# Performance work log

Hardware: AMD Instinct MI355X
Metric: run time of the kernel (lower is better)

## Reference

```python
import jax, jax.numpy as jnp
import numpy as np

SEGMENT_LENGTHS = [1024, 4096]
DILATION_RATES = [1, 2]
HILBERT_CHUNK = 4096
B, N, H, D = 2, 4096, 16, 64


def _hilbert_mapping(n: int) -> np.ndarray:
    """Replicates _generate_hilbert_curve: gather indices for a length-n chunk."""
    if n <= 64:
        return np.arange(n, dtype=np.int64)
    size = 1
    while size * size < n:
        size *= 2

    def d2xy(nn, d):
        x = y = 0
        s = 1
        while s < nn:
            rx = 1 if (d // 2) & 1 else 0
            ry = 1 if (d ^ rx) & 1 else 0
            if ry == 0:
                if rx == 1:
                    x, y = nn - 1 - x, nn - 1 - y
                x, y = y, x
            x += s * rx
            y += s * ry
            d //= 4
            s *= 2
        return x, y

    mapping = np.zeros(n, dtype=np.int64)
    h2l = {}
    for i in range(min(n, size * size)):
        x, y = d2xy(size, i)
        li = y * size + x
        if li < n:
            h2l[i] = li
    hidx = 0
    for i in sorted(h2l):
        mapping[h2l[i]] = hidx
        hidx += 1
    return mapping


def _apply_hilbert(t: jnp.ndarray) -> jnp.ndarray:
    # t: [b, n, h, d]; reorder sequence within HILBERT_CHUNK-sized chunks.
    n = t.shape[1]
    chunks = []
    for start in range(0, n, HILBERT_CHUNK):
        end = min(start + HILBERT_CHUNK, n)
        m = jnp.asarray(_hilbert_mapping(end - start))
        chunks.append(t[:, start:end][:, m])
    return jnp.concatenate(chunks, axis=1) if len(chunks) > 1 else chunks[0]


def _dilation_indices(s: int, r: int, offset: int) -> np.ndarray:
    # Replicates _create_dilation_pattern
    idx = np.arange(offset, s, r, dtype=np.int64)
    expected = (s + r - 1 - offset) // r
    if idx.shape[0] > expected:
        idx = idx[:expected]
    elif idx.shape[0] < expected:
        pad = np.arange(expected - idx.shape[0], dtype=np.int64) % idx.shape[0]
        idx = np.concatenate([idx, idx[pad]])
    return idx


def _dilated_attention(q, k, v):
    # LongNet-style dilated attention: heads partitioned across groups;
    # each group attends within segments over dilated positions.
    b, n, h, d = q.shape
    G = len(SEGMENT_LENGTHS)
    hg = h // G
    scale = 1.0 / np.sqrt(d).astype(np.float32)
    out = jnp.zeros_like(q)
    for g, (s, r) in enumerate(zip(SEGMENT_LENGTHS, DILATION_RATES)):
        offset = g % r
        idx = jnp.asarray(_dilation_indices(s, r, offset))
        hs = slice(g * hg, (g + 1) * hg)
        # [b, n//s, s, hg, d] -> dilated [b, n//s, s/r, hg, d]
        qg = q[:, :, hs].reshape(b, n // s, s, hg, d)[:, :, idx]
        kg = k[:, :, hs].reshape(b, n // s, s, hg, d)[:, :, idx]
        vg = v[:, :, hs].reshape(b, n // s, s, hg, d)[:, :, idx]
        att = jnp.einsum('bgqhd,bgkhd->bghqk', qg, kg) * scale
        att = jax.nn.softmax(att, axis=-1)
        og = jnp.einsum('bghqk,bgkhd->bgqhd', att, vg)
        full = jnp.zeros((b, n // s, s, hg, d), q.dtype).at[:, :, idx].set(og)
        out = out.at[:, :, hs].set(full.reshape(b, n, hg, d))
    return out


def setup_inputs() -> dict:
    key = jax.random.key(0)
    kq, kk, kv = jax.random.split(key, 3)
    q = jax.random.normal(kq, (B, N, H, D), dtype=jnp.float32)
    k = jax.random.normal(kk, (B, N, H, D), dtype=jnp.float32)
    v = jax.random.normal(kv, (B, N, H, D), dtype=jnp.float32)
    return {'q': q, 'k': k, 'v': v}


def reference(q, k, v):
    k_h = _apply_hilbert(k)
    v_h = _apply_hilbert(v)
    return _dilated_attention(q, k_h, v_h)
```

## Files before the change

### kernel.cpp

```cpp
#include <hip/hip_runtime.h>
#include <hip/hip_bf16.h>

#define N_ 4096
#define H_ 16
#define D_ 64
#define G1ROWOFF 65536

typedef __attribute__((ext_vector_type(4))) float f32x4;
typedef __attribute__((ext_vector_type(8))) _Float16 f16x8;

#define AS1 __attribute__((address_space(1)))
#define AS3 __attribute__((address_space(3)))

__device__ __forceinline__ unsigned int pkrtz(float a, float b){
  auto h = __builtin_amdgcn_cvt_pkrtz(a, b);
  unsigned int r; __builtin_memcpy(&r, &h, 4); return r;
}
__device__ __forceinline__ unsigned int pku(unsigned int lo, unsigned int hi){
  return lo | (hi << 16);
}

__global__ __launch_bounds__(1024) void hilbert_map_kernel(int* __restrict__ mapping){
  __shared__ int sm[4096];
  const int t = threadIdx.x;
#pragma unroll
  for(int jj=0;jj<4;jj++) mapping[t*4+jj] = 0;
  int li_a[4], val_a[4];
#pragma unroll
  for(int jj=0;jj<4;jj++){
    int i = t*4+jj;
    int x=0,y=0,d=i;
#pragma unroll
    for(int s=1;s<64;s<<=1){
      int rx=(d>>1)&1;
      int ry=(d^rx)&1;
      if(ry==0){
        if(rx==1){ x=63-x; y=63-y; }
        int tp=x; x=y; y=tp;
      }
      x+=s*rx; y+=s*ry;
      d>>=2;
    }
    int li=y*64+x;
    li_a[jj]=li;
    val_a[jj]=(li<4096)?1:0;
    sm[i]=val_a[jj];
  }
  __syncthreads();
  for(int off=1;off<4096;off<<=1){
    int v[4];
#pragma unroll
    for(int jj=0;jj<4;jj++){
      int i=t*4+jj;
      v[jj]=sm[i]+((i>=off)?sm[i-off]:0);
    }
    __syncthreads();
#pragma unroll
    for(int jj=0;jj<4;jj++) sm[t*4+jj]=v[jj];
    __syncthreads();
  }
#pragma unroll
  for(int jj=0;jj<4;jj++){
    if(val_a[jj]){
      int rank=sm[t*4+jj]-1;
      int li=li_a[jj];
      int wi=(li>=0)?li:(4096+li);
      if(wi>=0 && wi<4096) atomicMax(&mapping[wi], rank);
    }
  }
}

__global__ __launch_bounds__(256) void prep_kv_kernel(
    const float* __restrict__ K, const float* __restrict__ V,
    const int* __restrict__ hmap,
    unsigned short* __restrict__ Kh, unsigned short* __restrict__ Vt)
{
  __shared__ unsigned short Vlds[64*72];
  const int bid = blockIdx.x, tid = threadIdx.x;
  int b, h, dstRowBase, srcRow;
  const int r = tid>>2, part = tid&3;
  if (bid < 1024){
    int t64 = bid&63; h = (bid>>6)&7; b = bid>>9;
    dstRowBase = (b*8+h)*4096 + t64*64;
    srcRow = t64*64 + r;
  } else {
    int bid2 = bid-1024;
    int t64 = bid2&31; int h8 = (bid2>>5)&7; b = bid2>>8; h = 8+h8;
    dstRowBase = G1ROWOFF + (b*8+h8)*2048 + t64*64;
    srcRow = 1 + 2*(t64*64 + r);
  }
  const int src = hmap[srcRow];
  const size_t sb = (((size_t)(b*N_+src))*H_ + h)*D_ + part*16;
  {
    const float4* kp = (const float4*)(K + sb);
    float4 a=kp[0], c=kp[1], e=kp[2], g=kp[3];
    uint4 w0, w1;
    w0.x=pkrtz(a.x,a.y); w0.y=pkrtz(a.z,a.w); w0.z=pkrtz(c.x,c.y); w0.w=pkrtz(c.z,c.w);
    w1.x=pkrtz(e.x,e.y); w1.y=pkrtz(e.z,e.w); w1.z=pkrtz(g.x,g.y); w1.w=pkrtz(g.z,g.w);
    char* dst = (char*)Kh + ((size_t)(dstRowBase+r))*128;
    *(uint4*)(dst + ((2*part  )^(r&7))*16) = w0;
    *(uint4*)(dst + ((2*part+1)^(r&7))*16) = w1;
  }
  {
    const float4* vp = (const float4*)(V + sb);
    float4 a=vp[0], c=vp[1], e=vp[2], g=vp[3];
    uint4 w0, w1;
    w0.x=pkrtz(a.x,a.y); w0.y=pkrtz(a.z,a.w); w0.z=pkrtz(c.x,c.y); w0.w=pkrtz(c.z,c.w);
    w1.x=pkrtz(e.x,e.y); w1.y=pkrtz(e.z,e.w); w1.z=pkrtz(g.x,g.y); w1.w=pkrtz(g.z,g.w);
    uint4* dst=(uint4*)&Vlds[r*72 + part*16];
    dst[0]=w0; dst[1]=w1;
  }
  __syncthreads();
  {
    const int d = tid>>2, p2 = tid&3;
    unsigned int w0[4], w1[4];
#pragma unroll
    for(int c=0;c<2;c++){
      int kb = 32*c + 4*p2;
      unsigned int* w = c ? w1 : w0;
      w[0] = pku(Vlds[(kb+ 0)*72+d], Vlds[(kb+ 1)*72+d]);
      w[1] = pku(Vlds[(kb+ 2)*72+d], Vlds[(kb+ 3)*72+d]);
      w[2] = pku(Vlds[(kb+16)*72+d], Vlds[(kb+17)*72+d]);
      w[3] = pku(Vlds[(kb+18)*72+d], Vlds[(kb+19)*72+d]);
    }
    char* dst = (char*)Vt + ((size_t)(dstRowBase+d))*128;
    *(uint4*)(dst + ((p2  )^(d&7))*16) = *(uint4*)w0;
    *(uint4*)(dst + ((p2+4)^(d&7))*16) = *(uint4*)w1;
  }
}

__global__ __launch_bounds__(256, 2) void dilated_attn_kernel(
    const float* __restrict__ Q, const unsigned short* __restrict__ Kh,
    const unsigned short* __restrict__ Vt, float* __restrict__ Out)
{
  __shared__ __align__(16) char smem[65536];

  const int bid = blockIdx.x, tid = threadIdx.x;
  const int wave = tid>>6, lane = tid&63;
  const int lr = lane&15, lg = lane>>4;

  int b, outH, qstep, qoff, njobs, nrj;
  int qloc[2];
  size_t kb0, kb1;
  if (bid < 256){
    int xcd = bid&7, idx = bid>>3;
    int kblk = idx&15, Hp = idx>>4;
    int H = xcd + 8*Hp;
    b = H>>3; outH = 8 + (H&7);
    qstep = 2; qoff = 1; njobs = 1; nrj = 16;
    qloc[0] = kblk*128; qloc[1] = qloc[0];
    size_t rowBase = (size_t)G1ROWOFF + (size_t)H*2048;
    kb0 = rowBase*128; kb1 = kb0 + 16*8192;
    int i = tid>>1, half = tid&1;
    int zpos = 2*(qloc[0] + i);
    float4 z = {0.f,0.f,0.f,0.f};
    float4* op = (float4*)(Out + (((size_t)(b*N_+zpos))*H_ + outH)*D_ + half*32);
#pragma unroll
    for(int j=0;j<8;j++) op[j]=z;
  } else {
    int p = bid - 256;
    int xcd = p&7, idx = p>>3;
    int pair = idx&3, Gp = idx>>2;
    int G = xcd + 8*Gp;
    b = G>>5; int seg=(G>>3)&3; int h=G&7; outH=h;
    qstep = 1; qoff = 0; njobs = 2; nrj = 8;
    qloc[0] = seg*1024 + pair*128;
    qloc[1] = seg*1024 + (pair+4)*128;
    size_t rowBase = ((size_t)(b*8+h))*4096 + (size_t)seg*1024;
    kb0 = rowBase*128; kb1 = kb0;
  }

  const float SCL = 0.125f * 1.4426950408889634f;
  f16x8 qf[2][2];
  f32x4 acc[2][4];
  f32x4 accl[2];
  const f32x4 FZ = {0.f,0.f,0.f,0.f};
  union{ unsigned int u[4]; f16x8 v; } ONES;
  ONES.u[0]=0x3C003C00u; ONES.u[1]=0x3C003C00u; ONES.u[2]=0x3C003C00u; ONES.u[3]=0x3C003C00u;

  auto loadQ = [&](int ql0){
#pragma unroll
    for(int qs=0;qs<2;qs++){
      int qpos = qoff + qstep*(ql0 + wave*32 + qs*16 + lr);
      const float* qp = Q + (((size_t)(b*N_+qpos))*H_ + outH)*D_;
#pragma unroll
      for(int dc=0;dc<2;dc++){
        float4 a = *(const float4*)(qp + dc*32 + lg*8);
        float4 c = *(const float4*)(qp + dc*32 + lg*8 + 4);
        union{ unsigned int u[4]; f16x8 v; } pk;
        pk.u[0]=pkrtz(a.x*SCL,a.y*SCL); pk.u[1]=pkrtz(a.z*SCL,a.w*SCL);
        pk.u[2]=pkrtz(c.x*SCL,c.y*SCL); pk.u[3]=pkrtz(c.z*SCL,c.w*SCL);
        qf[qs][dc]=pk.v;
      }
    }
  };

  const int swz = lr&7;
  const int kA0 = lr*128 + ((  lg)^swz)*16;
  const int kA1 = lr*128 + ((4+lg)^swz)*16;
  const int vA0 = 8192 + lr*128 + ((  lg)^swz)*16;
  const int vA1 = 8192 + lr*128 + ((4+lg)^swz)*16;

  const char* gBase = (wave<2) ? (const char*)Kh : (const char*)Vt;
  const int sOff = (tid&127)*16;
  const int sHalf = (wave<2) ? 0 : 8192;
  auto stage = [&](int bufOff, int t){
    size_t off = ((t>=16)? kb1 : kb0) + (size_t)(t&15)*8192 + sOff;
    const char* gsrc = gBase + off;
    char* ldst = smem + bufOff + sHalf + sOff;
#pragma unroll
    for(int i=0;i<4;i++){
      __builtin_amdgcn_global_load_lds((const AS1 void*)(gsrc + i*2048),
                                       (AS3 void*)(ldst + i*2048), 16, 0, 0);
    }
  };

  auto epilogue = [&](int ql0){
#pragma unroll
    for(int qs=0;qs<2;qs++)
#pragma unroll
      for(int r=0;r<4;r++){
        float inv = 1.0f/accl[qs][r];
        int qpos = qoff + qstep*(ql0 + wave*32 + qs*16 + lg*4 + r);
        float* op = Out + (((size_t)(b*N_+qpos))*H_ + outH)*D_ + lr;
#pragma unroll
        for(int dt=0;dt<4;dt++) op[dt*16] = acc[qs][dt][r]*inv;
      }
  };

  stage(0, 0); stage(16384, 1);
  int p = 0;
  for(int j=0; j<njobs; ++j){
    loadQ(qloc[j]);
#pragma unroll
    for(int qs=0;qs<2;qs++){
#pragma unroll
      for(int dt=0;dt<4;dt++) acc[qs][dt] = FZ;
      accl[qs] = FZ;
    }
    for(int r=0; r<nrj; ++r, ++p){
      asm volatile("s_waitcnt vmcnt(0)" ::: "memory");
      __builtin_amdgcn_s_barrier();
      const int half = (p&1)*32768;
      if (p < 15){
        const int oth = ((p+1)&1)*32768;
        stage(oth, 2*p+2); stage(oth+16384, 2*p+3);
      }
      const char* smA = smem + half;
      const char* smB = smem + half + 16384;

      f32x4 sA[2][4], sB[2][4];
#pragma unroll
      for(int kt=0;kt<4;kt++){
        f16x8 k0 = *(const f16x8*)(smA + kA0 + kt*2048);
        f16x8 k1 = *(const f16x8*)(smA + kA1 + kt*2048);
#pragma unroll
        for(int qs=0;qs<2;qs++){
          sA[qs][kt] = __builtin_amdgcn_mfma_f32_16x16x32_f16(k0, qf[qs][0], FZ, 0,0,0);
          sA[qs][kt] = __builtin_amdgcn_mfma_f32_16x16x32_f16(k1, qf[qs][1], sA[qs][kt],0,0,0);
        }
      }

      unsigned int UA[2][4][2], UB[2][4][2];
#pragma unroll
      for(int kt=0;kt<4;kt++){
        f16x8 k0 = *(const f16x8*)(smB + kA0 + kt*2048);
        f16x8 k1 = *(const f16x8*)(smB + kA1 + kt*2048);
        sB[0][kt] = __builtin_amdgcn_mfma_f32_16x16x32_f16(k0, qf[0][0], FZ, 0,0,0);
        UA[0][kt][0] = pkrtz(__builtin_amdgcn_exp2f(sA[0][kt][0]),
                             __builtin_amdgcn_exp2f(sA[0][kt][1]));
        sB[0][kt] = __builtin_amdgcn_mfma_f32_16x16x32_f16(k1, qf[0][1], sB[0][kt],0,0,0);
        UA[0][kt][1] = pkrtz(__builtin_amdgcn_exp2f(sA[0][kt][2]),
                             __builtin_amdgcn_exp2f(sA[0][kt][3]));
        sB[1][kt] = __builtin_amdgcn_mfma_f32_16x16x32_f16(k0, qf[1][0], FZ, 0,0,0);
        UA[1][kt][0] = pkrtz(__builtin_amdgcn_exp2f(sA[1][kt][0]),
                             __builtin_amdgcn_exp2f(sA[1][kt][1]));
        sB[1][kt] = __builtin_amdgcn_mfma_f32_16x16x32_f16(k1, qf[1][1], sB[1][kt],0,0,0);
        UA[1][kt][1] = pkrtz(__builtin_amdgcn_exp2f(sA[1][kt][2]),
                             __builtin_amdgcn_exp2f(sA[1][kt][3]));
      }
      union{ unsigned int u[4]; f16x8 v; } pfA[2][2];
#pragma unroll
      for(int qs=0;qs<2;qs++)
#pragma unroll
        for(int c=0;c<2;c++){
          pfA[qs][c].u[0]=UA[qs][2*c][0]; pfA[qs][c].u[1]=UA[qs][2*c][1];
          pfA[qs][c].u[2]=UA[qs][2*c+1][0]; pfA[qs][c].u[3]=UA[qs][2*c+1][1];
        }

#pragma unroll
      for(int c=0;c<2;c++){
        const int vAc = c ? vA1 : vA0;
#pragma unroll
        for(int dt=0;dt<4;dt++){
          f16x8 vf = *(const f16x8*)(smA + vAc + dt*2048);
          const int bqs = dt>>1, bkt = 2*c + (dt&1);
          acc[0][dt] = __builtin_amdgcn_mfma_f32_16x16x32_f16(pfA[0][c].v, vf, acc[0][dt],0,0,0);
          UB[bqs][bkt][0] = pkrtz(__builtin_amdgcn_exp2f(sB[bqs][bkt][0]),
                                  __builtin_amdgcn_exp2f(sB[bqs][bkt][1]));
          acc[1][dt] = __builtin_amdgcn_mfma_f32_16x16x32_f16(pfA[1][c].v, vf, acc[1][dt],0,0,0);
          UB[bqs][bkt][1] = pkrtz(__builtin_amdgcn_exp2f(sB[bqs][bkt][2]),
                                  __builtin_amdgcn_exp2f(sB[bqs][bkt][3]));
        }
        accl[0] = __builtin_amdgcn_mfma_f32_16x16x32_f16(pfA[0][c].v, ONES.v, accl[0],0,0,0);
        accl[1] = __builtin_amdgcn_mfma_f32_16x16x32_f16(pfA[1][c].v, ONES.v, accl[1],0,0,0);
      }

#pragma unroll
      for(int c=0;c<2;c++){
        union{ unsigned int u[4]; f16x8 v; } pf0, pf1;
        pf0.u[0]=UB[0][2*c][0]; pf0.u[1]=UB[0][2*c][1]; pf0.u[2]=UB[0][2*c+1][0]; pf0.u[3]=UB[0][2*c+1][1];
        pf1.u[0]=UB[1][2*c][0]; pf1.u[1]=UB[1][2*c][1]; pf1.u[2]=UB[1][2*c+1][0]; pf1.u[3]=UB[1][2*c+1][1];
        const int vAc = c ? vA1 : vA0;
#pragma unroll
        for(int dt=0;dt<4;dt++){
          f16x8 vf = *(const f16x8*)(smB + vAc + dt*2048);
          acc[0][dt] = __builtin_amdgcn_mfma_f32_16x16x32_f16(pf0.v, vf, acc[0][dt],0,0,0);
          acc[1][dt] = __builtin_amdgcn_mfma_f32_16x16x32_f16(pf1.v, vf, acc[1][dt],0,0,0);
        }
        accl[0] = __builtin_amdgcn_mfma_f32_16x16x32_f16(pf0.v, ONES.v, accl[0],0,0,0);
        accl[1] = __builtin_amdgcn_mfma_f32_16x16x32_f16(pf1.v, ONES.v, accl[1],0,0,0);
      }
    }
    epilogue(qloc[j]);
  }
}

extern "C" void kernel_launch(void* const* d_in, const int* in_sizes, int n_in,
                              void* d_out, int out_size, void* d_ws, size_t ws_size,
                              hipStream_t stream){
  const float* Q = (const float*)d_in[0];
  const float* K = (const float*)d_in[1];
  const float* V = (const float*)d_in[2];
  float* Out = (float*)d_out;

  int* hmap = (int*)d_ws;
  unsigned short* Kh = (unsigned short*)((char*)d_ws + 16384);
  unsigned short* Vt = (unsigned short*)((char*)d_ws + 16384 + 12582912);

  hipLaunchKernelGGL(hilbert_map_kernel, dim3(1), dim3(1024), 0, stream, hmap);
  hipLaunchKernelGGL(prep_kv_kernel, dim3(1536), dim3(256), 0, stream, K, V, hmap, Kh, Vt);
  hipLaunchKernelGGL(dilated_attn_kernel, dim3(512), dim3(256), 0, stream, Q, Kh, Vt, Out);
}
```

Baseline: 67.70 us.

## Load V fragments directly from global into registers, stage only K in LDS

```diff
diff --git a/kernel.cpp b/kernel.cpp
--- a/kernel.cpp
+++ b/kernel.cpp
@@ -133,7 +133,7 @@
     const float* __restrict__ Q, const unsigned short* __restrict__ Kh,
     const unsigned short* __restrict__ Vt, float* __restrict__ Out)
 {
-  __shared__ __align__(16) char smem[65536];
+  __shared__ __align__(16) char smem[32768];
 
   const int bid = blockIdx.x, tid = threadIdx.x;
   const int wave = tid>>6, lane = tid&63;
@@ -198,20 +198,18 @@
   const int swz = lr&7;
   const int kA0 = lr*128 + ((  lg)^swz)*16;
   const int kA1 = lr*128 + ((4+lg)^swz)*16;
-  const int vA0 = 8192 + lr*128 + ((  lg)^swz)*16;
-  const int vA1 = 8192 + lr*128 + ((4+lg)^swz)*16;
-
-  const char* gBase = (wave<2) ? (const char*)Kh : (const char*)Vt;
-  const int sOff = (tid&127)*16;
-  const int sHalf = (wave<2) ? 0 : 8192;
-  auto stage = [&](int bufOff, int t){
-    size_t off = ((t>=16)? kb1 : kb0) + (size_t)(t&15)*8192 + sOff;
-    const char* gsrc = gBase + off;
-    char* ldst = smem + bufOff + sHalf + sOff;
-#pragma unroll
-    for(int i=0;i<4;i++){
-      __builtin_amdgcn_global_load_lds((const AS1 void*)(gsrc + i*2048),
-                                       (AS3 void*)(ldst + i*2048), 16, 0, 0);
+  const int vG0 = lr*128 + ((  lg)^swz)*16;
+  const int vG1 = lr*128 + ((4+lg)^swz)*16;
+
+  const int stW = wave*2048 + lane*16;
+  auto stageK = [&](int bufOff, int t){
+    size_t off = ((t>=16)? kb1 : kb0) + (size_t)(t&15)*8192 + stW;
+    const char* gsrc = (const char*)Kh + off;
+    char* ldst = smem + bufOff + stW;
+#pragma unroll
+    for(int i=0;i<2;i++){
+      __builtin_amdgcn_global_load_lds((const AS1 void*)(gsrc + i*1024),
+                                       (AS3 void*)(ldst + i*1024), 16, 0, 0);
     }
   };
 
@@ -228,7 +226,7 @@
       }
   };
 
-  stage(0, 0); stage(16384, 1);
+  stageK(0, 0); stageK(8192, 1);
   int p = 0;
   for(int j=0; j<njobs; ++j){
     loadQ(qloc[j]);
@@ -241,13 +239,27 @@
     for(int r=0; r<nrj; ++r, ++p){
       asm volatile("s_waitcnt vmcnt(0)" ::: "memory");
       __builtin_amdgcn_s_barrier();
-      const int half = (p&1)*32768;
+      const int half = (p&1)*16384;
       if (p < 15){
-        const int oth = ((p+1)&1)*32768;
-        stage(oth, 2*p+2); stage(oth+16384, 2*p+3);
+        const int oth = ((p+1)&1)*16384;
+        stageK(oth, 2*p+2); stageK(oth+8192, 2*p+3);
       }
       const char* smA = smem + half;
-      const char* smB = smem + half + 16384;
+      const char* smB = smem + half + 8192;
+
+      const int tA = 2*p, tB = 2*p+1;
+      const char* gVA = (const char*)Vt + ((tA>=16)? kb1 : kb0) + (size_t)(tA&15)*8192;
+      const char* gVB = (const char*)Vt + ((tB>=16)? kb1 : kb0) + (size_t)(tB&15)*8192;
+      uint4 vfA[2][4], vfB[2][4];
+#pragma unroll
+      for(int c=0;c<2;c++){
+        const int vGc = c ? vG1 : vG0;
+#pragma unroll
+        for(int dt=0;dt<4;dt++){
+          vfA[c][dt] = *(const uint4*)(gVA + vGc + dt*2048);
+          vfB[c][dt] = *(const uint4*)(gVB + vGc + dt*2048);
+        }
+      }
 
       f32x4 sA[2][4], sB[2][4];
 #pragma unroll
@@ -290,10 +302,9 @@
 
 #pragma unroll
       for(int c=0;c<2;c++){
-        const int vAc = c ? vA1 : vA0;
 #pragma unroll
         for(int dt=0;dt<4;dt++){
-          f16x8 vf = *(const f16x8*)(smA + vAc + dt*2048);
+          f16x8 vf; __builtin_memcpy(&vf, &vfA[c][dt], 16);
           const int bqs = dt>>1, bkt = 2*c + (dt&1);
           acc[0][dt] = __builtin_amdgcn_mfma_f32_16x16x32_f16(pfA[0][c].v, vf, acc[0][dt],0,0,0);
           UB[bqs][bkt][0] = pkrtz(__builtin_amdgcn_exp2f(sB[bqs][bkt][0]),
@@ -311,10 +322,9 @@
         union{ unsigned int u[4]; f16x8 v; } pf0, pf1;
         pf0.u[0]=UB[0][2*c][0]; pf0.u[1]=UB[0][2*c][1]; pf0.u[2]=UB[0][2*c+1][0]; pf0.u[3]=UB[0][2*c+1][1];
         pf1.u[0]=UB[1][2*c][0]; pf1.u[1]=UB[1][2*c][1]; pf1.u[2]=UB[1][2*c+1][0]; pf1.u[3]=UB[1][2*c+1][1];
-        const int vAc = c ? vA1 : vA0;
 #pragma unroll
         for(int dt=0;dt<4;dt++){
-          f16x8 vf = *(const f16x8*)(smB + vAc + dt*2048);
+          f16x8 vf; __builtin_memcpy(&vf, &vfB[c][dt], 16);
           acc[0][dt] = __builtin_amdgcn_mfma_f32_16x16x32_f16(pf0.v, vf, acc[0][dt],0,0,0);
           acc[1][dt] = __builtin_amdgcn_mfma_f32_16x16x32_f16(pf1.v, vf, acc[1][dt],0,0,0);
         }
```

After: 70.84 us. 1.05x slower.
